# Kernel optimization log

Measured on AMD Instinct MI355X. Metric: run time of the kernel, lower is better.

Reference implementation:

```python
import jax, jax.numpy as jnp
import numpy as np

N_HEAD = 16


def setup_inputs() -> dict:
    key = jax.random.key(0)
    ks = jax.random.split(key, 9)
    B, T, C = 4, 2048, 1024
    s = 1.0 / np.sqrt(C)
    x = jax.random.normal(ks[0], (B, T, C), dtype=jnp.float32)
    Wq = jax.random.normal(ks[1], (C, C), dtype=jnp.float32) * s
    bq = jax.random.normal(ks[2], (C,), dtype=jnp.float32) * 0.01
    Wk = jax.random.normal(ks[3], (C, C), dtype=jnp.float32) * s
    bk = jax.random.normal(ks[4], (C,), dtype=jnp.float32) * 0.01
    Wv = jax.random.normal(ks[5], (C, C), dtype=jnp.float32) * s
    bv = jax.random.normal(ks[6], (C,), dtype=jnp.float32) * 0.01
    Wp = jax.random.normal(ks[7], (C, C), dtype=jnp.float32) * s
    bp = jax.random.normal(ks[8], (C,), dtype=jnp.float32) * 0.01
    return {"x": x, "Wq": Wq, "bq": bq, "Wk": Wk, "bk": bk,
            "Wv": Wv, "bv": bv, "Wp": Wp, "bp": bp}


def reference(x, Wq, bq, Wk, bk, Wv, bv, Wp, bp):
    B, T, C = x.shape
    H = N_HEAD
    d = C // H
    # projections (torch Linear: x @ W.T + b)
    q = (x @ Wq.T + bq).reshape(B, T, H, d)  # [B,T,H,d]
    k = (x @ Wk.T + bk).reshape(B, T, H, d)
    v = (x @ Wv.T + bv).reshape(B, T, H, d)
    scale = 1.0 / jnp.sqrt(jnp.asarray(d, dtype=x.dtype))
    # scores: [B,H,T,T]
    att = jnp.einsum('bqhd,bkhd->bhqk', q, k) * scale
    causal = jnp.tril(jnp.ones((T, T), dtype=bool))  # [T,T]
    att = jnp.where(causal[None, None], att, jnp.asarray(-jnp.inf, dtype=att.dtype))
    att = jax.nn.softmax(att, axis=-1)
    y = jnp.einsum('bhqk,bkhd->bqhd', att, v).reshape(B, T, C)
    return y @ Wp.T + bp
```

## Files before the change

### kernel.cpp

```cpp
#include <hip/hip_runtime.h>
#include <hip/hip_bf16.h>

typedef __attribute__((ext_vector_type(8))) short bf16x8;
typedef __attribute__((ext_vector_type(4))) float f32x4;

static constexpr int Tt = 2048;
static constexpr int Cc = 1024;
static constexpr int Dd = 64;
static constexpr int Mm = 8192;

static constexpr size_t XN = (size_t)Mm * Cc;
static constexpr size_t WN = (size_t)Cc * Cc;

__device__ __forceinline__ void async_copy16(void* lds, const void* g) {
  __builtin_amdgcn_global_load_lds(
      (const __attribute__((address_space(1))) void*)g,
      (__attribute__((address_space(3))) void*)lds, 16, 0, 0);
}

__device__ __forceinline__ unsigned short f2bf(float f) {
  union { float f; unsigned int u; } v; v.f = f;
  unsigned int r = (v.u + 0x7fffu + ((v.u >> 16) & 1u)) >> 16;
  return (unsigned short)r;
}
__device__ __forceinline__ unsigned int pack2bf(float f0, float f1) {
  unsigned int b0 = __float_as_uint(f0) + 0x8000u;
  unsigned int b1 = __float_as_uint(f1) + 0x8000u;
  return (b1 & 0xffff0000u) | (b0 >> 16);
}
__device__ __forceinline__ unsigned int cvtpk2bf(float f0, float f1) {
  unsigned int r;
  asm("v_cvt_pk_bf16_f32 %0, %1, %2" : "=v"(r) : "v"(f0), "v"(f1));
  return r;
}
__device__ __forceinline__ uint4 ldconv_f32(const float* p) {
  float4 lo = *(const float4*)p;
  float4 hi = *(const float4*)(p + 4);
  uint4 r;
  r.x = pack2bf(lo.x, lo.y);
  r.y = pack2bf(lo.z, lo.w);
  r.z = pack2bf(hi.x, hi.y);
  r.w = pack2bf(hi.z, hi.w);
  return r;
}

__global__ __launch_bounds__(256) void convert_all(
    const float* __restrict__ x, const float* __restrict__ wq,
    const float* __restrict__ wk, const float* __restrict__ wv,
    unsigned short* __restrict__ dst,
    const float* __restrict__ wp, unsigned short* __restrict__ wpb)
{
  if (blockIdx.x >= 5632) {
    const size_t i = ((size_t)(blockIdx.x - 5632) * 256 + threadIdx.x) * 8;
    *(uint4*)(wpb + i) = ldconv_f32(wp + i);
    return;
  }
  const size_t i = ((size_t)blockIdx.x * 256 + threadIdx.x) * 8;
  const float* s; size_t off;
  if (i < XN)                { s = x;  off = 0; }
  else if (i < XN + WN)      { s = wq; off = XN; }
  else if (i < XN + 2 * WN)  { s = wk; off = XN + WN; }
  else                       { s = wv; off = XN + 2 * WN; }
  *(uint4*)(dst + i) = ldconv_f32(s + (i - off));
}

template <int MODE>
__device__ __forceinline__ void gemm_async_body(
    unsigned short* As, unsigned short* Bs,
    const unsigned short* __restrict__ A,
    const unsigned short* __restrict__ Bt,
    const float* __restrict__ bias,
    unsigned short* __restrict__ out, float mult)
{
  const int tid  = threadIdx.x;
  const int wave = tid >> 6;
  const int lane = tid & 63;
  const int m16  = lane & 15;
  const int quad = lane >> 4;
  const int row0 = blockIdx.x * 128;
  const int col0 = blockIdx.y * 128;
  const int wm = (wave >> 1) * 64;
  const int wn = (wave & 1) * 64;

  f32x4 acc[4][4] = {};

  const unsigned short* Ag[4];
  const unsigned short* Bg[4];
#pragma unroll
  for (int j = 0; j < 4; ++j) {
    const int c  = j * 256 + tid;
    const int rw = c >> 3;
    const int sw = (c & 7) ^ (rw & 7);
    Ag[j] = A  + (size_t)(row0 + rw) * Cc + sw * 8;
    Bg[j] = Bt + (size_t)(col0 + rw) * Cc + sw * 8;
  }

  for (int k0 = 0; k0 < Cc; k0 += 64) {
    __syncthreads();
#pragma unroll
    for (int j = 0; j < 4; ++j)
      async_copy16((char*)As + j * 4096 + wave * 1024, Ag[j] + k0);
#pragma unroll
    for (int j = 0; j < 4; ++j)
      async_copy16((char*)Bs + j * 4096 + wave * 1024, Bg[j] + k0);
    __syncthreads();
#pragma unroll
    for (int kk = 0; kk < 2; ++kk) {
      const int chp = (kk * 4 + quad) ^ (m16 & 7);
      bf16x8 af[4], bfr[4];
#pragma unroll
      for (int i = 0; i < 4; ++i)
        af[i] = *(const bf16x8*)(As + (wm + i * 16 + m16) * 64 + chp * 8);
#pragma unroll
      for (int j = 0; j < 4; ++j)
        bfr[j] = *(const bf16x8*)(Bs + (wn + j * 16 + m16) * 64 + chp * 8);
#pragma unroll
      for (int i = 0; i < 4; ++i)
#pragma unroll
        for (int j = 0; j < 4; ++j)
          acc[i][j] = __builtin_amdgcn_mfma_f32_16x16x32_bf16(af[i], bfr[j], acc[i][j], 0, 0, 0);
    }
  }

  float bvj[4];
#pragma unroll
  for (int j = 0; j < 4; ++j)
    bvj[j] = bias[col0 + wn + j * 16 + m16];
#pragma unroll
  for (int i = 0; i < 4; ++i) {
    const int rbase = row0 + wm + i * 16 + quad * 4;
#pragma unroll
    for (int j = 0; j < 4; ++j) {
      const int col = col0 + wn + j * 16 + m16;
      const float bv = bvj[j];
      if (MODE == 0) {
#pragma unroll
        for (int r = 0; r < 4; ++r)
          out[(size_t)(rbase + r) * Cc + col] = f2bf((acc[i][j][r] + bv) * mult);
      } else if (MODE == 1) {
        const int t0 = rbase & (Tt - 1);
        const int b  = rbase >> 11;
        ushort4 pk;
        pk.x = f2bf(acc[i][j][0] + bv);
        pk.y = f2bf(acc[i][j][1] + bv);
        pk.z = f2bf(acc[i][j][2] + bv);
        pk.w = f2bf(acc[i][j][3] + bv);
        *(ushort4*)(out + (size_t)(b * Cc + col) * Tt + t0) = pk;
      } else {
        float* outf = (float*)out;
#pragma unroll
        for (int r = 0; r < 4; ++r)
          outf[(size_t)(rbase + r) * Cc + col] = acc[i][j][r] + bv;
      }
    }
  }
}

__global__ __launch_bounds__(256) void qkv_gemm(
    const unsigned short* __restrict__ Xb,
    const unsigned short* __restrict__ Wqb, const float* __restrict__ bq,
    const unsigned short* __restrict__ Wkb, const float* __restrict__ bk,
    const unsigned short* __restrict__ Wvb, const float* __restrict__ bv,
    unsigned short* Qw, unsigned short* Kw, unsigned short* Vtw)
{
  __shared__ __align__(16) unsigned short smem[16384];
  const int z = blockIdx.z;
  if (z == 0)      gemm_async_body<0>(smem, smem + 8192, Xb, Wqb, bq, Qw, 0.125f * 1.44269504f);
  else if (z == 1) gemm_async_body<0>(smem, smem + 8192, Xb, Wkb, bk, Kw, 1.0f);
  else             gemm_async_body<1>(smem, smem + 8192, Xb, Wvb, bv, Vtw, 1.0f);
}

__global__ __launch_bounds__(256) void proj_gemm_pre(
    const unsigned short* __restrict__ Yb,
    const unsigned short* __restrict__ Wpb, const float* __restrict__ bp,
    float* __restrict__ out)
{
  __shared__ __align__(16) unsigned short smem[16384];
  gemm_async_body<2>(smem, smem + 8192, Yb, Wpb, bp, (unsigned short*)out, 1.0f);
}

__global__ __launch_bounds__(256) void attn_pair(
    const unsigned short* __restrict__ Q,
    const unsigned short* __restrict__ Kg,
    const unsigned short* __restrict__ Vt,
    unsigned short* __restrict__ Y)
{
  __shared__ __align__(16) unsigned short KV[2 * 8192];

  const int tid  = threadIdx.x;
  const int wave = tid >> 6;
  const int lane = tid & 63;
  const int m16  = lane & 15;
  const int quad = lane >> 4;

  const int bh = blockIdx.x;
  const int p  = blockIdx.y;
  const int b = bh >> 4, h = bh & 15;

  const unsigned short* Kb = Kg + (size_t)(b * Tt) * Cc + h * Dd;
  const unsigned short* Vb = Vt + (size_t)(b * Cc + h * Dd) * Tt;

  const int maxH = 32 - 2 * p;
  const int TOT  = 34;
  const int chp  = quad ^ ((m16 >> 1) & 3);

  bf16x8 onesA;
#pragma unroll
  for (int i = 0; i < 8; ++i) onesA[i] = (short)0x3F80;

  const unsigned short* pK[2];
  const unsigned short* pV[2];
#pragma unroll
  for (int ii = 0; ii < 2; ++ii) {
    const int cc  = ii * 256 + tid;
    const int kkS = cc >> 8;
    const int rrS = (cc >> 2) & 63;
    const int chd = (cc & 3) ^ ((rrS >> 1) & 3);
    pK[ii] = Kb + (size_t)rrS * Cc + kkS * 32 + chd * 8;
    pV[ii] = Vb + (size_t)rrS * Tt + kkS * 32 + chd * 8;
  }
  const unsigned short* pK0[2] = {pK[0], pK[1]};
  const unsigned short* pV0[2] = {pV[0], pV[1]};

  int sidx = 63 - 4 * p - wave;
  int qw = sidx * 32;
  int nk = (sidx >> 1) + 1;
  bf16x8 qf[2][2];
  {
    const unsigned short* Qb = Q + (size_t)(b * Tt + qw) * Cc + h * Dd;
#pragma unroll
    for (int s = 0; s < 2; ++s)
#pragma unroll
      for (int kk = 0; kk < 2; ++kk)
        qf[s][kk] = *(const bf16x8*)(Qb + (size_t)(s * 16 + m16) * Cc + kk * 32 + quad * 8);
  }
  f32x4 o[2][4] = {};
  f32x4 lz[2] = {};

  auto writeout = [&](int qw_) {
#pragma unroll
    for (int s = 0; s < 2; ++s) {
      const float l = lz[s][0];
      const float inv = (l > 0.f) ? (1.0f / l) : 0.f;
      const int t = qw_ + s * 16 + m16;
      unsigned short* yp = Y + (size_t)(b * Tt + t) * Cc + h * Dd + quad * 4;
#pragma unroll
      for (int jn = 0; jn < 4; ++jn) {
        uint2 pk;
        pk.x = cvtpk2bf(o[s][jn][0] * inv, o[s][jn][1] * inv);
        pk.y = cvtpk2bf(o[s][jn][2] * inv, o[s][jn][3] * inv);
        *(uint2*)(yp + jn * 16) = pk;
      }
    }
  };

  {
    char* KbufB = (char*)KV;
    char* VbufB = KbufB + 8192;
#pragma unroll
    for (int ii = 0; ii < 2; ++ii) {
      async_copy16(KbufB + ii * 4096 + wave * 1024, pK[ii]);
      async_copy16(VbufB + ii * 4096 + wave * 1024, pV[ii]);
    }
#pragma unroll
    for (int ii = 0; ii < 2; ++ii) { pK[ii] += 64 * Cc; pV[ii] += 64; }
  }

  for (int g = 0; g < TOT; ++g) {
    if (g == maxH) {
      writeout(qw);
      sidx = 4 * p + wave;
      qw = sidx * 32;
      nk = (sidx >> 1) + 1;
      const unsigned short* Qb = Q + (size_t)(b * Tt + qw) * Cc + h * Dd;
#pragma unroll
      for (int s = 0; s < 2; ++s) {
#pragma unroll
        for (int kk = 0; kk < 2; ++kk)
          qf[s][kk] = *(const bf16x8*)(Qb + (size_t)(s * 16 + m16) * Cc + kk * 32 + quad * 8);
#pragma unroll
        for (int jn = 0; jn < 4; ++jn)
          o[s][jn] = f32x4{0.f, 0.f, 0.f, 0.f};
        lz[s] = f32x4{0.f, 0.f, 0.f, 0.f};
      }
    }
    const int kt  = (g < maxH) ? g : g - maxH;
    const int k0  = kt * 64;
    const int buf = g & 1;

    __syncthreads();
    if (g + 1 < TOT) {
      if (g + 1 == maxH) {
#pragma unroll
        for (int ii = 0; ii < 2; ++ii) { pK[ii] = pK0[ii]; pV[ii] = pV0[ii]; }
      }
      char* KbufB = (char*)KV + (buf ^ 1) * 16384;
      char* VbufB = KbufB + 8192;
#pragma unroll
      for (int ii = 0; ii < 2; ++ii) {
        async_copy16(KbufB + ii * 4096 + wave * 1024, pK[ii]);
        async_copy16(VbufB + ii * 4096 + wave * 1024, pV[ii]);
      }
#pragma unroll
      for (int ii = 0; ii < 2; ++ii) { pK[ii] += 64 * Cc; pV[ii] += 64; }
    }

    if (kt < nk) {
      const unsigned short* Kbuf = KV + buf * 8192;
      const unsigned short* Vbuf = Kbuf + 4096;
      bf16x8 kf[2][4], vf[2][4];
#pragma unroll
      for (int kk = 0; kk < 2; ++kk)
#pragma unroll
        for (int jn = 0; jn < 4; ++jn) {
          kf[kk][jn] = *(const bf16x8*)(Kbuf + kk * 2048 + (jn * 16 + m16) * 32 + chp * 8);
          vf[kk][jn] = *(const bf16x8*)(Vbuf + kk * 2048 + (jn * 16 + m16) * 32 + chp * 8);
        }

#pragma unroll
      for (int s = 0; s < 2; ++s) {
        const int smin = qw + s * 16;
        if (k0 > smin + 15) continue;
        f32x4 sv[4] = {};
        __builtin_amdgcn_s_setprio(1);
#pragma unroll
        for (int kk = 0; kk < 2; ++kk)
#pragma unroll
          for (int jn = 0; jn < 4; ++jn)
            sv[jn] = __builtin_amdgcn_mfma_f32_16x16x32_bf16(kf[kk][jn], qf[s][kk], sv[jn], 0, 0, 0);
        __builtin_amdgcn_s_setprio(0);

        if (k0 + 63 <= smin) {
#pragma unroll
          for (int jn = 0; jn < 4; ++jn)
#pragma unroll
            for (int r = 0; r < 4; ++r)
              sv[jn][r] = __builtin_exp2f(sv[jn][r]);
        } else {
          const int qcol = smin + m16;
#pragma unroll
          for (int jn = 0; jn < 4; ++jn)
#pragma unroll
            for (int r = 0; r < 4; ++r)
              sv[jn][r] = (k0 + jn * 16 + quad * 4 + r > qcol)
                              ? 0.f : __builtin_exp2f(sv[jn][r]);
        }

        unsigned int P2[4][2];
#pragma unroll
        for (int jn = 0; jn < 4; ++jn) {
          P2[jn][0] = cvtpk2bf(sv[jn][0], sv[jn][1]);
          P2[jn][1] = cvtpk2bf(sv[jn][2], sv[jn][3]);
        }
#pragma unroll
        for (int kk = 0; kk < 2; ++kk) {
          auto r0 = __builtin_amdgcn_permlane32_swap(P2[2 * kk][0], P2[2 * kk + 1][0], false, false);
          auto t0 = __builtin_amdgcn_permlane16_swap(r0[0], r0[1], false, false);
          auto r1 = __builtin_amdgcn_permlane32_swap(P2[2 * kk][1], P2[2 * kk + 1][1], false, false);
          auto t1 = __builtin_amdgcn_permlane16_swap(r1[0], r1[1], false, false);
          uint4 u;
          u.x = t0[0];
          u.y = t1[0];
          u.z = t0[1];
          u.w = t1[1];
          union { uint4 u4; bf16x8 bf; } cv; cv.u4 = u;
          __builtin_amdgcn_s_setprio(1);
          lz[s] = __builtin_amdgcn_mfma_f32_16x16x32_bf16(onesA, cv.bf, lz[s], 0, 0, 0);
#pragma unroll
          for (int jn = 0; jn < 4; ++jn)
            o[s][jn] = __builtin_amdgcn_mfma_f32_16x16x32_bf16(vf[kk][jn], cv.bf, o[s][jn], 0, 0, 0);
          __builtin_amdgcn_s_setprio(0);
        }
      }
    }
  }

  writeout(qw);
}

__global__ __launch_bounds__(256) void proj_gemm(
    const unsigned short* __restrict__ Y,
    const float* __restrict__ Wp, const float* __restrict__ bp,
    float* __restrict__ out)
{
  __shared__ __align__(16) unsigned short As[8192];
  __shared__ __align__(16) unsigned short Bs[8192];
  const int tid  = threadIdx.x;
  const int wave = tid >> 6;
  const int lane = tid & 63;
  const int m16  = lane & 15;
  const int quad = lane >> 4;
  const int row0 = blockIdx.x * 128;
  const int col0 = blockIdx.y * 128;
  const int wm = (wave >> 1) * 64;
  const int wn = (wave & 1) * 64;
  const int chp = quad ^ ((m16 >> 1) & 3);

  f32x4 acc[4][4] = {};

  const int c0 = tid, c1 = 256 + tid;
  const int sw0 = (c0 & 3) ^ ((c0 >> 3) & 3);
  const int sw1 = (c1 & 3) ^ ((c1 >> 3) & 3);
  const unsigned short* Ag0 = Y + (size_t)(row0 + (c0 >> 2)) * Cc + sw0 * 8;
  const unsigned short* Ag1 = Y + (size_t)(row0 + (c1 >> 2)) * Cc + sw1 * 8;
  const float* Bg0 = Wp + (size_t)(col0 + (c0 >> 2)) * Cc + (c0 & 3) * 8;
  const float* Bg1 = Wp + (size_t)(col0 + (c1 >> 2)) * Cc + (c1 & 3) * 8;
  const int bd0 = ((c0 >> 2) * 4 + sw0) * 8;
  const int bd1 = ((c1 >> 2) * 4 + sw1) * 8;

  uint4 b0 = ldconv_f32(Bg0);
  uint4 b1 = ldconv_f32(Bg1);

  async_copy16((char*)As + wave * 1024,        Ag0);
  async_copy16((char*)As + 4096 + wave * 1024, Ag1);
  *(uint4*)(Bs + bd0) = b0;
  *(uint4*)(Bs + bd1) = b1;
  b0 = ldconv_f32(Bg0 + 32);
  b1 = ldconv_f32(Bg1 + 32);

  int buf = 0;
  for (int k0 = 0; k0 < Cc; k0 += 32) {
    __syncthreads();
    if (k0 + 32 < Cc) {
      char* Ab = (char*)As + (buf ^ 1) * 8192;
      async_copy16(Ab + wave * 1024,        Ag0 + k0 + 32);
      async_copy16(Ab + 4096 + wave * 1024, Ag1 + k0 + 32);
      *(uint4*)(Bs + (buf ^ 1) * 4096 + bd0) = b0;
      *(uint4*)(Bs + (buf ^ 1) * 4096 + bd1) = b1;
      if (k0 + 64 < Cc) {
        b0 = ldconv_f32(Bg0 + k0 + 64);
        b1 = ldconv_f32(Bg1 + k0 + 64);
      }
    }
    const unsigned short* Asb = As + buf * 4096;
    const unsigned short* Bsb = Bs + buf * 4096;
    bf16x8 af[4], bfr[4];
#pragma unroll
    for (int i = 0; i < 4; ++i)
      af[i] = *(const bf16x8*)(Asb + (wm + i * 16 + m16) * 32 + chp * 8);
#pragma unroll
    for (int j = 0; j < 4; ++j)
      bfr[j] = *(const bf16x8*)(Bsb + (wn + j * 16 + m16) * 32 + chp * 8);
#pragma unroll
    for (int i = 0; i < 4; ++i)
#pragma unroll
      for (int j = 0; j < 4; ++j)
        acc[i][j] = __builtin_amdgcn_mfma_f32_16x16x32_bf16(af[i], bfr[j], acc[i][j], 0, 0, 0);
    buf ^= 1;
  }

#pragma unroll
  for (int i = 0; i < 4; ++i) {
    const int rbase = row0 + wm + i * 16 + quad * 4;
#pragma unroll
    for (int j = 0; j < 4; ++j) {
      const int col = col0 + wn + j * 16 + m16;
      const float bv = bp[col];
#pragma unroll
      for (int r = 0; r < 4; ++r)
        out[(size_t)(rbase + r) * Cc + col] = acc[i][j][r] + bv;
    }
  }
}

extern "C" void kernel_launch(void* const* d_in, const int* in_sizes, int n_in,
                              void* d_out, int out_size, void* d_ws, size_t ws_size,
                              hipStream_t stream)
{
  const float* x  = (const float*)d_in[0];
  const float* Wq = (const float*)d_in[1];
  const float* bq = (const float*)d_in[2];
  const float* Wk = (const float*)d_in[3];
  const float* bk = (const float*)d_in[4];
  const float* Wv = (const float*)d_in[5];
  const float* bv = (const float*)d_in[6];
  const float* Wp = (const float*)d_in[7];
  const float* bp = (const float*)d_in[8];

  unsigned short* ws  = (unsigned short*)d_ws;
  unsigned short* Qw  = ws;
  unsigned short* Kw  = ws + (size_t)1 * XN;
  unsigned short* Vtw = ws + (size_t)2 * XN;
  unsigned short* Yw  = ws + (size_t)3 * XN;
  unsigned short* Wpb = ws + (size_t)4 * XN;
  const bool pre = ws_size >= ((size_t)4 * XN + WN) * sizeof(unsigned short);

  unsigned short* cvt = (unsigned short*)d_out;
  unsigned short* Xb  = cvt;
  unsigned short* Wqb = cvt + XN;
  unsigned short* Wkb = cvt + XN + WN;
  unsigned short* Wvb = cvt + XN + 2 * WN;
  float* out = (float*)d_out;

  convert_all<<<pre ? 6144 : 5632, 256, 0, stream>>>(x, Wq, Wk, Wv, cvt, Wp, Wpb);
  qkv_gemm<<<dim3(64, 8, 3), 256, 0, stream>>>(Xb, Wqb, bq, Wkb, bk, Wvb, bv, Qw, Kw, Vtw);
  attn_pair<<<dim3(64, 8), 256, 0, stream>>>(Qw, Kw, Vtw, Yw);
  if (pre) proj_gemm_pre<<<dim3(64, 8), 256, 0, stream>>>(Yw, Wpb, bp, out);
  else     proj_gemm<<<dim3(64, 8), 256, 0, stream>>>(Yw, Wp, bp, out);
}
```

Baseline: 251.8 us.

## Split attention into 16-row query strips with doubled grid

The attention kernel now gives each wave one 16-row query strip instead of a 32-row strip (two 16-row sub-strips), and launches twice as many blocks (grid y 16 instead of 8). Causal pairing of a high and a low strip per block is kept, so each block runs 33 key tiles. This doubles the number of blocks to fill more CUs and cuts per-wave register use. In exchange, each K/V tile loaded into LDS is reused by half as many query rows, so global and LDS traffic per FLOP rises.

```diff
diff --git a/kernel.cpp b/kernel.cpp
--- a/kernel.cpp
+++ b/kernel.cpp
@@ -179,7 +179,7 @@
   gemm_async_body<2>(smem, smem + 8192, Yb, Wpb, bp, (unsigned short*)out, 1.0f);
 }
 
-__global__ __launch_bounds__(256) void attn_pair(
+__global__ __launch_bounds__(256) void attn_strip16(
     const unsigned short* __restrict__ Q,
     const unsigned short* __restrict__ Kg,
     const unsigned short* __restrict__ Vt,
@@ -200,8 +200,8 @@
   const unsigned short* Kb = Kg + (size_t)(b * Tt) * Cc + h * Dd;
   const unsigned short* Vb = Vt + (size_t)(b * Cc + h * Dd) * Tt;
 
-  const int maxH = 32 - 2 * p;
-  const int TOT  = 34;
+  const int maxH = 32 - p;
+  const int TOT  = 33;
   const int chp  = quad ^ ((m16 >> 1) & 3);
 
   bf16x8 onesA;
@@ -222,35 +222,27 @@
   const unsigned short* pK0[2] = {pK[0], pK[1]};
   const unsigned short* pV0[2] = {pV[0], pV[1]};
 
-  int sidx = 63 - 4 * p - wave;
-  int qw = sidx * 32;
-  int nk = (sidx >> 1) + 1;
-  bf16x8 qf[2][2];
+  int qw = (127 - 4 * p - wave) * 16;
+  bf16x8 qf[2];
   {
-    const unsigned short* Qb = Q + (size_t)(b * Tt + qw) * Cc + h * Dd;
-#pragma unroll
-    for (int s = 0; s < 2; ++s)
-#pragma unroll
-      for (int kk = 0; kk < 2; ++kk)
-        qf[s][kk] = *(const bf16x8*)(Qb + (size_t)(s * 16 + m16) * Cc + kk * 32 + quad * 8);
-  }
-  f32x4 o[2][4] = {};
-  f32x4 lz[2] = {};
+    const unsigned short* Qb = Q + (size_t)(b * Tt + qw + m16) * Cc + h * Dd;
+#pragma unroll
+    for (int kk = 0; kk < 2; ++kk)
+      qf[kk] = *(const bf16x8*)(Qb + kk * 32 + quad * 8);
+  }
+  f32x4 o[4] = {};
+  f32x4 lz = {};
 
   auto writeout = [&](int qw_) {
-#pragma unroll
-    for (int s = 0; s < 2; ++s) {
-      const float l = lz[s][0];
-      const float inv = (l > 0.f) ? (1.0f / l) : 0.f;
-      const int t = qw_ + s * 16 + m16;
-      unsigned short* yp = Y + (size_t)(b * Tt + t) * Cc + h * Dd + quad * 4;
-#pragma unroll
-      for (int jn = 0; jn < 4; ++jn) {
-        uint2 pk;
-        pk.x = cvtpk2bf(o[s][jn][0] * inv, o[s][jn][1] * inv);
-        pk.y = cvtpk2bf(o[s][jn][2] * inv, o[s][jn][3] * inv);
-        *(uint2*)(yp + jn * 16) = pk;
-      }
+    const float l = lz[0];
+    const float inv = (l > 0.f) ? (1.0f / l) : 0.f;
+    unsigned short* yp = Y + (size_t)(b * Tt + qw_ + m16) * Cc + h * Dd + quad * 4;
+#pragma unroll
+    for (int jn = 0; jn < 4; ++jn) {
+      uint2 pk;
+      pk.x = cvtpk2bf(o[jn][0] * inv, o[jn][1] * inv);
+      pk.y = cvtpk2bf(o[jn][2] * inv, o[jn][3] * inv);
+      *(uint2*)(yp + jn * 16) = pk;
     }
   };
 
@@ -269,20 +261,15 @@
   for (int g = 0; g < TOT; ++g) {
     if (g == maxH) {
       writeout(qw);
-      sidx = 4 * p + wave;
-      qw = sidx * 32;
-      nk = (sidx >> 1) + 1;
-      const unsigned short* Qb = Q + (size_t)(b * Tt + qw) * Cc + h * Dd;
-#pragma unroll
-      for (int s = 0; s < 2; ++s) {
-#pragma unroll
-        for (int kk = 0; kk < 2; ++kk)
-          qf[s][kk] = *(const bf16x8*)(Qb + (size_t)(s * 16 + m16) * Cc + kk * 32 + quad * 8);
-#pragma unroll
-        for (int jn = 0; jn < 4; ++jn)
-          o[s][jn] = f32x4{0.f, 0.f, 0.f, 0.f};
-        lz[s] = f32x4{0.f, 0.f, 0.f, 0.f};
-      }
+      qw = (4 * p + wave) * 16;
+      const unsigned short* Qb = Q + (size_t)(b * Tt + qw + m16) * Cc + h * Dd;
+#pragma unroll
+      for (int kk = 0; kk < 2; ++kk)
+        qf[kk] = *(const bf16x8*)(Qb + kk * 32 + quad * 8);
+#pragma unroll
+      for (int jn = 0; jn < 4; ++jn)
+        o[jn] = f32x4{0.f, 0.f, 0.f, 0.f};
+      lz = f32x4{0.f, 0.f, 0.f, 0.f};
     }
     const int kt  = (g < maxH) ? g : g - maxH;
     const int k0  = kt * 64;
@@ -305,73 +292,67 @@
       for (int ii = 0; ii < 2; ++ii) { pK[ii] += 64 * Cc; pV[ii] += 64; }
     }
 
-    if (kt < nk) {
-      const unsigned short* Kbuf = KV + buf * 8192;
-      const unsigned short* Vbuf = Kbuf + 4096;
-      bf16x8 kf[2][4], vf[2][4];
-#pragma unroll
-      for (int kk = 0; kk < 2; ++kk)
-#pragma unroll
-        for (int jn = 0; jn < 4; ++jn) {
-          kf[kk][jn] = *(const bf16x8*)(Kbuf + kk * 2048 + (jn * 16 + m16) * 32 + chp * 8);
-          vf[kk][jn] = *(const bf16x8*)(Vbuf + kk * 2048 + (jn * 16 + m16) * 32 + chp * 8);
-        }
-
-#pragma unroll
-      for (int s = 0; s < 2; ++s) {
-        const int smin = qw + s * 16;
-        if (k0 > smin + 15) continue;
-        f32x4 sv[4] = {};
-        __builtin_amdgcn_s_setprio(1);
-#pragma unroll
-        for (int kk = 0; kk < 2; ++kk)
-#pragma unroll
-          for (int jn = 0; jn < 4; ++jn)
-            sv[jn] = __builtin_amdgcn_mfma_f32_16x16x32_bf16(kf[kk][jn], qf[s][kk], sv[jn], 0, 0, 0);
-        __builtin_amdgcn_s_setprio(0);
-
-        if (k0 + 63 <= smin) {
-#pragma unroll
-          for (int jn = 0; jn < 4; ++jn)
-#pragma unroll
-            for (int r = 0; r < 4; ++r)
-              sv[jn][r] = __builtin_exp2f(sv[jn][r]);
-        } else {
-          const int qcol = smin + m16;
-#pragma unroll
-          for (int jn = 0; jn < 4; ++jn)
-#pragma unroll
-            for (int r = 0; r < 4; ++r)
-              sv[jn][r] = (k0 + jn * 16 + quad * 4 + r > qcol)
-                              ? 0.f : __builtin_exp2f(sv[jn][r]);
-        }
-
-        unsigned int P2[4][2];
-#pragma unroll
-        for (int jn = 0; jn < 4; ++jn) {
-          P2[jn][0] = cvtpk2bf(sv[jn][0], sv[jn][1]);
-          P2[jn][1] = cvtpk2bf(sv[jn][2], sv[jn][3]);
-        }
-#pragma unroll
-        for (int kk = 0; kk < 2; ++kk) {
-          auto r0 = __builtin_amdgcn_permlane32_swap(P2[2 * kk][0], P2[2 * kk + 1][0], false, false);
-          auto t0 = __builtin_amdgcn_permlane16_swap(r0[0], r0[1], false, false);
-          auto r1 = __builtin_amdgcn_permlane32_swap(P2[2 * kk][1], P2[2 * kk + 1][1], false, false);
-          auto t1 = __builtin_amdgcn_permlane16_swap(r1[0], r1[1], false, false);
-          uint4 u;
-          u.x = t0[0];
-          u.y = t1[0];
-          u.z = t0[1];
-          u.w = t1[1];
-          union { uint4 u4; bf16x8 bf; } cv; cv.u4 = u;
-          __builtin_amdgcn_s_setprio(1);
-          lz[s] = __builtin_amdgcn_mfma_f32_16x16x32_bf16(onesA, cv.bf, lz[s], 0, 0, 0);
-#pragma unroll
-          for (int jn = 0; jn < 4; ++jn)
-            o[s][jn] = __builtin_amdgcn_mfma_f32_16x16x32_bf16(vf[kk][jn], cv.bf, o[s][jn], 0, 0, 0);
-          __builtin_amdgcn_s_setprio(0);
-        }
+    const unsigned short* Kbuf = KV + buf * 8192;
+    const unsigned short* Vbuf = Kbuf + 4096;
+    bf16x8 kf[2][4], vf[2][4];
+#pragma unroll
+    for (int kk = 0; kk < 2; ++kk)
+#pragma unroll
+      for (int jn = 0; jn < 4; ++jn) {
+        kf[kk][jn] = *(const bf16x8*)(Kbuf + kk * 2048 + (jn * 16 + m16) * 32 + chp * 8);
+        vf[kk][jn] = *(const bf16x8*)(Vbuf + kk * 2048 + (jn * 16 + m16) * 32 + chp * 8);
       }
+
+    const int smin = qw;
+    f32x4 sv[4] = {};
+    __builtin_amdgcn_s_setprio(1);
+#pragma unroll
+    for (int kk = 0; kk < 2; ++kk)
+#pragma unroll
+      for (int jn = 0; jn < 4; ++jn)
+        sv[jn] = __builtin_amdgcn_mfma_f32_16x16x32_bf16(kf[kk][jn], qf[kk], sv[jn], 0, 0, 0);
+    __builtin_amdgcn_s_setprio(0);
+
+    if (k0 + 63 <= smin) {
+#pragma unroll
+      for (int jn = 0; jn < 4; ++jn)
+#pragma unroll
+        for (int r = 0; r < 4; ++r)
+          sv[jn][r] = __builtin_exp2f(sv[jn][r]);
+    } else {
+      const int qcol = smin + m16;
+#pragma unroll
+      for (int jn = 0; jn < 4; ++jn)
+#pragma unroll
+        for (int r = 0; r < 4; ++r)
+          sv[jn][r] = (k0 + jn * 16 + quad * 4 + r > qcol)
+                          ? 0.f : __builtin_exp2f(sv[jn][r]);
+    }
+
+    unsigned int P2[4][2];
+#pragma unroll
+    for (int jn = 0; jn < 4; ++jn) {
+      P2[jn][0] = cvtpk2bf(sv[jn][0], sv[jn][1]);
+      P2[jn][1] = cvtpk2bf(sv[jn][2], sv[jn][3]);
+    }
+#pragma unroll
+    for (int kk = 0; kk < 2; ++kk) {
+      auto r0 = __builtin_amdgcn_permlane32_swap(P2[2 * kk][0], P2[2 * kk + 1][0], false, false);
+      auto t0 = __builtin_amdgcn_permlane16_swap(r0[0], r0[1], false, false);
+      auto r1 = __builtin_amdgcn_permlane32_swap(P2[2 * kk][1], P2[2 * kk + 1][1], false, false);
+      auto t1 = __builtin_amdgcn_permlane16_swap(r1[0], r1[1], false, false);
+      uint4 u;
+      u.x = t0[0];
+      u.y = t1[0];
+      u.z = t0[1];
+      u.w = t1[1];
+      union { uint4 u4; bf16x8 bf; } cv; cv.u4 = u;
+      __builtin_amdgcn_s_setprio(1);
+      lz = __builtin_amdgcn_mfma_f32_16x16x32_bf16(onesA, cv.bf, lz, 0, 0, 0);
+#pragma unroll
+      for (int jn = 0; jn < 4; ++jn)
+        o[jn] = __builtin_amdgcn_mfma_f32_16x16x32_bf16(vf[kk][jn], cv.bf, o[jn], 0, 0, 0);
+      __builtin_amdgcn_s_setprio(0);
     }
   }
 
@@ -494,7 +475,7 @@
 
   convert_all<<<pre ? 6144 : 5632, 256, 0, stream>>>(x, Wq, Wk, Wv, cvt, Wp, Wpb);
   qkv_gemm<<<dim3(64, 8, 3), 256, 0, stream>>>(Xb, Wqb, bq, Wkb, bk, Wvb, bv, Qw, Kw, Vtw);
-  attn_pair<<<dim3(64, 8), 256, 0, stream>>>(Qw, Kw, Vtw, Yw);
+  attn_strip16<<<dim3(64, 16), 256, 0, stream>>>(Qw, Kw, Vtw, Yw);
   if (pre) proj_gemm_pre<<<dim3(64, 8), 256, 0, stream>>>(Yw, Wpb, bp, out);
   else     proj_gemm<<<dim3(64, 8), 256, 0, stream>>>(Yw, Wp, bp, out);
 }
```

Measured after the change: 254.9 us. About the same (+1.2%).
